# Optimization experiments

Hardware: AMD Instinct MI355X
Metric: run time of the kernel (lower is better)

The kernel has to match this reference:

```python
import jax, jax.numpy as jnp
import numpy as np

EPS = 1e-5

def layer_norm(x, g, b):
    m = x.mean(-1, keepdims=True)
    v = ((x - m) ** 2).mean(-1, keepdims=True)
    return (x - m) * jax.lax.rsqrt(v + EPS) * g + b

def setup_inputs() -> dict:
    key = jax.random.key(0)
    ks = jax.random.split(key, 12)
    H = 2048; E = 2048; I = 2048; N = 32
    A = (H + E) // 2  # attention hidden = 2048
    s = lambda fan: 1.0 / np.sqrt(fan)
    inp = {
        "input":   jax.random.normal(ks[0], (I,), jnp.float32),
        "hiddens": jax.random.normal(ks[1], (N, H), jnp.float32),
        "cells":   jax.random.normal(ks[2], (N, H), jnp.float32),
        "external":jax.random.normal(ks[3], (E,), jnp.float32),
        # weights (torch nn.Linear layout: [out, in]); LN enabled -> no biases on linears
        "W_ai":   jax.random.uniform(ks[4], (A, H + E), jnp.float32, -s(H+E), s(H+E)),
        "W_attn": jax.random.uniform(ks[5], (1, A), jnp.float32, -s(A), s(A)),
        "W_merge":jax.random.uniform(ks[6], (H, H), jnp.float32, -s(H), s(H)),
        "W_iou":  jax.random.uniform(ks[7], (3 * H, I + H), jnp.float32, -s(I+H), s(I+H)),
        "W_fi":   jax.random.uniform(ks[8], (H, I), jnp.float32, -s(I), s(I)),
        "W_fh":   jax.random.uniform(ks[9], (H, H), jnp.float32, -s(H), s(H)),
        "g_merge": jnp.ones((H,), jnp.float32), "b_merge": jnp.zeros((H,), jnp.float32),
        "g_f": jnp.ones((H,), jnp.float32), "b_f": jnp.zeros((H,), jnp.float32),
        "g_i": jnp.ones((H,), jnp.float32), "b_i": jnp.zeros((H,), jnp.float32),
        "g_o": jnp.ones((H,), jnp.float32), "b_o": jnp.zeros((H,), jnp.float32),
        "g_u": jnp.ones((H,), jnp.float32), "b_u": jnp.zeros((H,), jnp.float32),
        "g_c": jnp.ones((H,), jnp.float32), "b_c": jnp.zeros((H,), jnp.float32),
    }
    return inp

def reference(input, hiddens, cells, external,
              W_ai, W_attn, W_merge, W_iou, W_fi, W_fh,
              g_merge, b_merge, g_f, b_f, g_i, b_i, g_o, b_o, g_u, b_u, g_c, b_c):
    N, H = hiddens.shape
    # forget-gate preactivations: [H] + [N,H] -> [N,H]
    f_lin = input @ W_fi.T + hiddens @ W_fh.T
    # attentive merge over children
    ext = jnp.broadcast_to(external, (N, external.shape[0]))
    ai = jnp.tanh(jnp.concatenate([hiddens, ext], axis=1) @ W_ai.T)       # [N, (H+E)//2]
    attn = jax.nn.softmax(ai @ W_attn.T, axis=0)                          # [N, 1]
    merged = (hiddens * attn).sum(0)                                      # [H]
    merge_hidden = jnp.tanh(layer_norm(merged @ W_merge.T, g_merge, b_merge))
    # i/o/u gates from [input ; merged_hidden]
    iou = jnp.concatenate([input, merge_hidden]) @ W_iou.T                # [3H]
    i_l, o_l, u_l = jnp.split(iou, 3)
    f = jax.nn.sigmoid(layer_norm(f_lin, g_f, b_f))                       # [N,H]
    i = jax.nn.sigmoid(layer_norm(i_l, g_i, b_i))
    o = jax.nn.sigmoid(layer_norm(o_l, g_o, b_o))
    u = jnp.tanh(layer_norm(u_l, g_u, b_u))                               # dropout=0 -> identity
    new_cell = layer_norm(i * u + (f * cells).sum(0), g_c, b_c)           # [H]
    new_h = o * jnp.tanh(new_cell)
    return new_h, new_cell
```

## Files before the change

### kernel.cpp

```cpp
#include <hip/hip_runtime.h>
#include <hip/hip_bf16.h>

typedef __bf16 bf16_t;
typedef __attribute__((ext_vector_type(8))) __bf16 bf16x8;
typedef __attribute__((ext_vector_type(4))) float f32x4;

#define EPSF 1e-5f

#define CVT8(dst, s0, s1)                                                      \
    dst[0]=(bf16_t)s0.x; dst[1]=(bf16_t)s0.y; dst[2]=(bf16_t)s0.z; dst[3]=(bf16_t)s0.w; \
    dst[4]=(bf16_t)s1.x; dst[5]=(bf16_t)s1.y; dst[6]=(bf16_t)s1.z; dst[7]=(bf16_t)s1.w;

__global__ __launch_bounds__(256) void s1(
    const float* __restrict__ hiddens, const float* __restrict__ external,
    const float* __restrict__ input,
    const float* __restrict__ W_ai, const float* __restrict__ W_fh,
    const float* __restrict__ W_fi, const float* __restrict__ W_attn,
    float* __restrict__ lp, float* __restrict__ fh_out, float* __restrict__ fi_out)
{
    __shared__ __align__(16) float sm[2176];
    const int b    = blockIdx.x;
    const int tid  = threadIdx.x;
    const int wave = tid >> 6;
    const int lane = tid & 63;

    if (b < 256) {
        const bool is_ai = (b < 128);
        const int  jt    = is_ai ? b : b - 128;
        const int  l15   = lane & 15;
        const int  quad  = lane >> 4;
        const int  k0    = wave * 512;
        const int  wstride = is_ai ? 4096 : 2048;
        const float* W  = is_ai ? W_ai : W_fh;

        const float* ap0 = hiddens + (size_t)l15 * 2048 + quad * 8 + k0;
        const float* ap1 = ap0 + 16 * 2048;
        const float* bp  = W + (size_t)(jt * 16 + l15) * wstride + quad * 8 + k0;

        f32x4 acc0 = {0.f,0.f,0.f,0.f}, acc1 = {0.f,0.f,0.f,0.f};

        if (is_ai) {
            const float* ep = bp + 2048;
            const float* xp = external + quad * 8 + k0;
            float ejacc = 0.f;
            for (int k = 0; k < 512; k += 32) {
                float4 b0 = *(const float4*)(bp + k);
                float4 b1 = *(const float4*)(bp + k + 4);
                float4 a0 = *(const float4*)(ap0 + k);
                float4 a1 = *(const float4*)(ap0 + k + 4);
                float4 c0 = *(const float4*)(ap1 + k);
                float4 c1 = *(const float4*)(ap1 + k + 4);
                bf16x8 bv, av0, av1;
                CVT8(bv, b0, b1); CVT8(av0, a0, a1); CVT8(av1, c0, c1);
                acc0 = __builtin_amdgcn_mfma_f32_16x16x32_bf16(av0, bv, acc0, 0, 0, 0);
                acc1 = __builtin_amdgcn_mfma_f32_16x16x32_bf16(av1, bv, acc1, 0, 0, 0);
                float4 e0 = *(const float4*)(ep + k);
                float4 e1 = *(const float4*)(ep + k + 4);
                float4 x0 = *(const float4*)(xp + k);
                float4 x1 = *(const float4*)(xp + k + 4);
                ejacc += e0.x*x0.x + e0.y*x0.y + e0.z*x0.z + e0.w*x0.w
                       + e1.x*x1.x + e1.y*x1.y + e1.z*x1.z + e1.w*x1.w;
            }
            ejacc += __shfl_xor(ejacc, 16, 64);
            ejacc += __shfl_xor(ejacc, 32, 64);
            if (quad == 0) sm[2048 + wave * 16 + l15] = ejacc;
        } else {
            for (int k = 0; k < 512; k += 32) {
                float4 b0 = *(const float4*)(bp + k);
                float4 b1 = *(const float4*)(bp + k + 4);
                float4 a0 = *(const float4*)(ap0 + k);
                float4 a1 = *(const float4*)(ap0 + k + 4);
                float4 c0 = *(const float4*)(ap1 + k);
                float4 c1 = *(const float4*)(ap1 + k + 4);
                bf16x8 bv, av0, av1;
                CVT8(bv, b0, b1); CVT8(av0, a0, a1); CVT8(av1, c0, c1);
                acc0 = __builtin_amdgcn_mfma_f32_16x16x32_bf16(av0, bv, acc0, 0, 0, 0);
                acc1 = __builtin_amdgcn_mfma_f32_16x16x32_bf16(av1, bv, acc1, 0, 0, 0);
            }
        }

        #pragma unroll
        for (int r = 0; r < 4; ++r) {
            sm[wave * 512 +       (quad * 4 + r) * 16 + l15] = acc0[r];
            sm[wave * 512 + 256 + (quad * 4 + r) * 16 + l15] = acc1[r];
        }
        __syncthreads();

        int row = tid >> 4, col = tid & 15;
        float s0  = sm[row*16+col]      + sm[512+row*16+col]
                  + sm[1024+row*16+col] + sm[1536+row*16+col];
        float s1v = sm[256+row*16+col]  + sm[768+row*16+col]
                  + sm[1280+row*16+col] + sm[1792+row*16+col];

        if (is_ai) {
            float ej = sm[2048+col] + sm[2064+col] + sm[2080+col] + sm[2096+col];
            float wat = W_attn[jt * 16 + col];
            float lg0 = tanhf(s0  + ej) * wat;
            float lg1 = tanhf(s1v + ej) * wat;
            #pragma unroll
            for (int m = 1; m < 16; m <<= 1) {
                lg0 += __shfl_xor(lg0, m, 64);
                lg1 += __shfl_xor(lg1, m, 64);
            }
            if (col == 0) {
                lp[jt * 32 + row]      = lg0;
                lp[jt * 32 + 16 + row] = lg1;
            }
        } else {
            fh_out[(size_t)row * 2048 + jt * 16 + col]        = s0;
            fh_out[(size_t)(16 + row) * 2048 + jt * 16 + col] = s1v;
        }
    } else {
        int bb = b - 256;
        #pragma unroll
        for (int r = 0; r < 2; ++r) {
            int row = bb * 8 + wave * 2 + r;
            const float4* wp = (const float4*)(W_fi + (size_t)row * 2048) + lane;
            const float4* xp = (const float4*)input + lane;
            float a = 0.f;
            #pragma unroll
            for (int k = 0; k < 512; k += 64) {
                float4 w = wp[k], v = xp[k];
                a += w.x*v.x + w.y*v.y + w.z*v.z + w.w*v.w;
            }
            #pragma unroll
            for (int off = 32; off; off >>= 1) a += __shfl_down(a, off, 64);
            if (lane == 0) fi_out[row] = a;
        }
    }
}

__global__ __launch_bounds__(256) void s2(
    const float* __restrict__ lp, const float* __restrict__ hiddens,
    const float* __restrict__ W_merge,
    const float* __restrict__ fi, const float* __restrict__ fh,
    float* __restrict__ mm, float* __restrict__ frs)
{
    int b = blockIdx.x, t = threadIdx.x;
    if (b < 256) {
        __shared__ float lred[32][9];
        __shared__ float attnw[32];
        __shared__ __align__(16) float merged_s[2048];
        int n = t >> 3, sl = t & 7;
        float p = 0.f;
        #pragma unroll
        for (int m = 0; m < 16; ++m) p += lp[(sl * 16 + m) * 32 + n];
        lred[n][sl] = p;
        __syncthreads();
        if (t < 32) {
            float lg = 0.f;
            #pragma unroll
            for (int m = 0; m < 8; ++m) lg += lred[t][m];
            lred[t][8] = lg;
        }
        __syncthreads();
        if (t < 32) {
            float mx = -1e30f;
            for (int m = 0; m < 32; ++m) mx = fmaxf(mx, lred[m][8]);
            float ss = 0.f;
            for (int m = 0; m < 32; ++m) ss += expf(lred[m][8] - mx);
            attnw[t] = expf(lred[t][8] - mx) / ss;
        }
        __syncthreads();
        #pragma unroll
        for (int i = 0; i < 8; ++i) {
            int h = i * 256 + t;
            float acc = 0.f;
            #pragma unroll 8
            for (int n2 = 0; n2 < 32; ++n2) acc += attnw[n2] * hiddens[n2 * 2048 + h];
            merged_s[h] = acc;
        }
        __syncthreads();

        int wave = t >> 6, lane = t & 63;
        #pragma unroll
        for (int r = 0; r < 2; ++r) {
            int row = b * 8 + wave * 2 + r;
            const float4* wp = (const float4*)(W_merge + (size_t)row * 2048) + lane;
            const float4* xp = (const float4*)merged_s + lane;
            float a = 0.f;
            #pragma unroll
            for (int k = 0; k < 512; k += 64) {
                float4 w = wp[k], v = xp[k];
                a += w.x*v.x + w.y*v.y + w.z*v.z + w.w*v.w;
            }
            #pragma unroll
            for (int off = 32; off; off >>= 1) a += __shfl_down(a, off, 64);
            if (lane == 0) mm[row] = a;
        }
    } else {
        __shared__ float s1a[256], s2a[256];
        int n = b - 256;
        float sum = 0.f, sq = 0.f;
        #pragma unroll
        for (int i = 0; i < 8; ++i) {
            int h = t * 8 + i;
            float v = fi[h] + fh[n * 2048 + h];
            sum += v; sq += v * v;
        }
        s1a[t] = sum; s2a[t] = sq;
        __syncthreads();
        for (int off = 128; off; off >>= 1) {
            if (t < off) { s1a[t] += s1a[t + off]; s2a[t] += s2a[t + off]; }
            __syncthreads();
        }
        if (t == 0) {
            const float inv = 1.f / 2048.f;
            float mean = s1a[0] * inv;
            frs[n * 2]     = mean;
            frs[n * 2 + 1] = rsqrtf(s2a[0] * inv - mean * mean + EPSF);
        }
    }
}

__global__ __launch_bounds__(256) void s3(
    const float* __restrict__ W_iou, const float* __restrict__ mm,
    const float* __restrict__ input, const float* __restrict__ g_merge,
    const float* __restrict__ b_merge,
    const float* __restrict__ fi, const float* __restrict__ fh,
    const float* __restrict__ frs, const float* __restrict__ g_f,
    const float* __restrict__ b_f, const float* __restrict__ cells,
    float* __restrict__ iou, float* __restrict__ fc)
{
    int b = blockIdx.x, t = threadIdx.x;
    if (b < 512) {
        __shared__ __align__(16) float xcat[4096];
        __shared__ float s1a[256], s2a[256];
        float v[8]; float sum = 0.f, sq = 0.f;
        #pragma unroll
        for (int i = 0; i < 8; ++i) {
            v[i] = mm[t * 8 + i]; sum += v[i]; sq += v[i] * v[i];
        }
        s1a[t] = sum; s2a[t] = sq;
        __syncthreads();
        for (int off = 128; off; off >>= 1) {
            if (t < off) { s1a[t] += s1a[t + off]; s2a[t] += s2a[t + off]; }
            __syncthreads();
        }
        const float inv = 1.f / 2048.f;
        float mean = s1a[0] * inv;
        float r = rsqrtf(s2a[0] * inv - mean * mean + EPSF);
        #pragma unroll
        for (int i = 0; i < 8; ++i) {
            int h = t * 8 + i;
            xcat[h]        = input[h];
            xcat[2048 + h] = tanhf((v[i] - mean) * r * g_merge[h] + b_merge[h]);
        }
        __syncthreads();

        int wave = t >> 6, lane = t & 63;
        #pragma unroll
        for (int rr = 0; rr < 3; ++rr) {
            int row = b * 12 + wave * 3 + rr;
            const float4* wp = (const float4*)(W_iou + (size_t)row * 4096) + lane;
            const float4* xp = (const float4*)xcat + lane;
            float a = 0.f;
            #pragma unroll
            for (int k = 0; k < 1024; k += 64) {
                float4 w = wp[k], x = xp[k];
                a += w.x*x.x + w.y*x.y + w.z*x.z + w.w*x.w;
            }
            #pragma unroll
            for (int off = 32; off; off >>= 1) a += __shfl_down(a, off, 64);
            if (lane == 0) iou[row] = a;
        }
    } else {
        int h = (b - 512) * 256 + t;
        float g = g_f[h], bb = b_f[h], f_i = fi[h];
        float acc = 0.f;
        for (int n = 0; n < 32; ++n) {
            float v = (f_i + fh[n * 2048 + h] - frs[n * 2]) * frs[n * 2 + 1] * g + bb;
            acc += (1.f / (1.f + expf(-v))) * cells[n * 2048 + h];
        }
        fc[h] = acc;
    }
}

__global__ __launch_bounds__(256) void s4_tail(
    const float* __restrict__ iou, const float* __restrict__ fc,
    const float* __restrict__ gi, const float* __restrict__ bi,
    const float* __restrict__ go, const float* __restrict__ bo,
    const float* __restrict__ gu, const float* __restrict__ bu,
    const float* __restrict__ gc, const float* __restrict__ bc,
    float* __restrict__ out)
{
    __shared__ float sA[6][256];
    int t = threadIdx.x;
    float vi[8], vo[8], vu[8];
    float si = 0, qi = 0, so = 0, qo = 0, su = 0, qu = 0;
    #pragma unroll
    for (int i = 0; i < 8; ++i) {
        int h = t * 8 + i;
        vi[i] = iou[h]; vo[i] = iou[2048 + h]; vu[i] = iou[4096 + h];
        si += vi[i]; qi += vi[i] * vi[i];
        so += vo[i]; qo += vo[i] * vo[i];
        su += vu[i]; qu += vu[i] * vu[i];
    }
    sA[0][t] = si; sA[1][t] = qi; sA[2][t] = so;
    sA[3][t] = qo; sA[4][t] = su; sA[5][t] = qu;
    __syncthreads();
    for (int off = 128; off; off >>= 1) {
        if (t < off) {
            #pragma unroll
            for (int c = 0; c < 6; ++c) sA[c][t] += sA[c][t + off];
        }
        __syncthreads();
    }
    const float inv = 1.f / 2048.f;
    float mi = sA[0][0] * inv, ri = rsqrtf(sA[1][0] * inv - mi * mi + EPSF);
    float mo = sA[2][0] * inv, ro = rsqrtf(sA[3][0] * inv - mo * mo + EPSF);
    float mu = sA[4][0] * inv, ru = rsqrtf(sA[5][0] * inv - mu * mu + EPSF);
    __syncthreads();

    float o_[8], v_[8];
    float sv = 0, qv = 0;
    #pragma unroll
    for (int i = 0; i < 8; ++i) {
        int h = t * 8 + i;
        float ivl = 1.f / (1.f + expf(-((vi[i] - mi) * ri * gi[h] + bi[h])));
        o_[i]     = 1.f / (1.f + expf(-((vo[i] - mo) * ro * go[h] + bo[h])));
        float uvl = tanhf((vu[i] - mu) * ru * gu[h] + bu[h]);
        v_[i] = ivl * uvl + fc[h];
        sv += v_[i]; qv += v_[i] * v_[i];
    }
    sA[0][t] = sv; sA[1][t] = qv;
    __syncthreads();
    for (int off = 128; off; off >>= 1) {
        if (t < off) { sA[0][t] += sA[0][t + off]; sA[1][t] += sA[1][t + off]; }
        __syncthreads();
    }
    float mc = sA[0][0] * inv, rc = rsqrtf(sA[1][0] * inv - mc * mc + EPSF);
    #pragma unroll
    for (int i = 0; i < 8; ++i) {
        int h = t * 8 + i;
        float nc = (v_[i] - mc) * rc * gc[h] + bc[h];
        out[h]        = o_[i] * tanhf(nc);
        out[2048 + h] = nc;
    }
}

extern "C" void kernel_launch(void* const* d_in, const int* in_sizes, int n_in,
                              void* d_out, int out_size, void* d_ws, size_t ws_size,
                              hipStream_t stream)
{
    const float* input    = (const float*)d_in[0];
    const float* hiddens  = (const float*)d_in[1];
    const float* cells    = (const float*)d_in[2];
    const float* external = (const float*)d_in[3];
    const float* W_ai     = (const float*)d_in[4];
    const float* W_attn   = (const float*)d_in[5];
    const float* W_merge  = (const float*)d_in[6];
    const float* W_iou    = (const float*)d_in[7];
    const float* W_fi     = (const float*)d_in[8];
    const float* W_fh     = (const float*)d_in[9];
    const float* g_merge  = (const float*)d_in[10];
    const float* b_merge  = (const float*)d_in[11];
    const float* g_f      = (const float*)d_in[12];
    const float* b_f      = (const float*)d_in[13];
    const float* g_i      = (const float*)d_in[14];
    const float* b_i      = (const float*)d_in[15];
    const float* g_o      = (const float*)d_in[16];
    const float* b_o      = (const float*)d_in[17];
    const float* g_u      = (const float*)d_in[18];
    const float* b_u      = (const float*)d_in[19];
    const float* g_c      = (const float*)d_in[20];
    const float* b_c      = (const float*)d_in[21];

    float* ws = (float*)d_ws;
    float* ws_lp     = ws;
    float* ws_fh     = ws + 4096;
    float* ws_fi     = ws + 69632;
    float* ws_frs    = ws + 71680;
    float* ws_mm     = ws + 71744;
    float* ws_fc     = ws + 73792;
    float* ws_iou    = ws + 75840;
    float* out = (float*)d_out;

    s1<<<512, 256, 0, stream>>>(hiddens, external, input, W_ai, W_fh, W_fi,
                                W_attn, ws_lp, ws_fh, ws_fi);
    s2<<<288, 256, 0, stream>>>(ws_lp, hiddens, W_merge, ws_fi, ws_fh,
                                ws_mm, ws_frs);
    s3<<<520, 256, 0, stream>>>(W_iou, ws_mm, input, g_merge, b_merge,
                                ws_fi, ws_fh, ws_frs, g_f, b_f, cells,
                                ws_iou, ws_fc);
    s4_tail<<<1, 256, 0, stream>>>(ws_iou, ws_fc, g_i, b_i, g_o, b_o,
                                   g_u, b_u, g_c, b_c, out);
}
```

Baseline: 286.9 us.

## Split attention merge into its own kernel and regroup forget-gate stats

Before, each of the 256 W_merge GEMV blocks redid the softmax over attention logits and the full 32x2048 weighted sum of hiddens. That work now runs once in a new 8-block kernel that writes the merged vector to workspace, and the GEMV reads it from global memory. The forget-gate layer-norm statistics move into the W_merge kernel's side blocks. Each of the 8 fc blocks computes all 32 row statistics itself and then builds fc, so the W_iou kernel no longer carries the fc blocks. This adds one kernel launch and repeats the statistics eight times, serially over 32 rows within each block, which may lengthen the critical path.

After: 312.7 us. 9.0% more time.

```diff
diff --git a/kernel.cpp b/kernel.cpp
--- a/kernel.cpp
+++ b/kernel.cpp
@@ -11,7 +11,7 @@
     dst[0]=(bf16_t)s0.x; dst[1]=(bf16_t)s0.y; dst[2]=(bf16_t)s0.z; dst[3]=(bf16_t)s0.w; \
     dst[4]=(bf16_t)s1.x; dst[5]=(bf16_t)s1.y; dst[6]=(bf16_t)s1.z; dst[7]=(bf16_t)s1.w;
 
-__global__ __launch_bounds__(256) void s1(
+__global__ __launch_bounds__(256) void k1(
     const float* __restrict__ hiddens, const float* __restrict__ external,
     const float* __restrict__ input,
     const float* __restrict__ W_ai, const float* __restrict__ W_fh,
@@ -130,54 +130,56 @@
     }
 }
 
-__global__ __launch_bounds__(256) void s2(
+__global__ __launch_bounds__(256) void k2(
     const float* __restrict__ lp, const float* __restrict__ hiddens,
-    const float* __restrict__ W_merge,
+    float* __restrict__ merged)
+{
+    __shared__ float lred[32][9];
+    __shared__ float attnw[32];
+    int b = blockIdx.x, t = threadIdx.x;
+    int n = t >> 3, sl = t & 7;
+    float p = 0.f;
+    #pragma unroll
+    for (int m = 0; m < 16; ++m) p += lp[(sl * 16 + m) * 32 + n];
+    lred[n][sl] = p;
+    __syncthreads();
+    if (t < 32) {
+        float lg = 0.f;
+        #pragma unroll
+        for (int m = 0; m < 8; ++m) lg += lred[t][m];
+        lred[t][8] = lg;
+    }
+    __syncthreads();
+    if (t < 32) {
+        float mx = -1e30f;
+        for (int m = 0; m < 32; ++m) mx = fmaxf(mx, lred[m][8]);
+        float ss = 0.f;
+        for (int m = 0; m < 32; ++m) ss += expf(lred[m][8] - mx);
+        attnw[t] = expf(lred[t][8] - mx) / ss;
+    }
+    __syncthreads();
+    int h = b * 256 + t;
+    float acc = 0.f;
+    #pragma unroll 8
+    for (int n2 = 0; n2 < 32; ++n2) acc += attnw[n2] * hiddens[n2 * 2048 + h];
+    merged[h] = acc;
+}
+
+__global__ __launch_bounds__(256) void k3(
+    const float* __restrict__ W_merge, const float* __restrict__ merged,
     const float* __restrict__ fi, const float* __restrict__ fh,
-    float* __restrict__ mm, float* __restrict__ frs)
+    const float* __restrict__ g_f, const float* __restrict__ b_f,
+    const float* __restrict__ cells,
+    float* __restrict__ mm, float* __restrict__ fc)
 {
     int b = blockIdx.x, t = threadIdx.x;
     if (b < 256) {
-        __shared__ float lred[32][9];
-        __shared__ float attnw[32];
-        __shared__ __align__(16) float merged_s[2048];
-        int n = t >> 3, sl = t & 7;
-        float p = 0.f;
-        #pragma unroll
-        for (int m = 0; m < 16; ++m) p += lp[(sl * 16 + m) * 32 + n];
-        lred[n][sl] = p;
-        __syncthreads();
-        if (t < 32) {
-            float lg = 0.f;
-            #pragma unroll
-            for (int m = 0; m < 8; ++m) lg += lred[t][m];
-            lred[t][8] = lg;
-        }
-        __syncthreads();
-        if (t < 32) {
-            float mx = -1e30f;
-            for (int m = 0; m < 32; ++m) mx = fmaxf(mx, lred[m][8]);
-            float ss = 0.f;
-            for (int m = 0; m < 32; ++m) ss += expf(lred[m][8] - mx);
-            attnw[t] = expf(lred[t][8] - mx) / ss;
-        }
-        __syncthreads();
-        #pragma unroll
-        for (int i = 0; i < 8; ++i) {
-            int h = i * 256 + t;
-            float acc = 0.f;
-            #pragma unroll 8
-            for (int n2 = 0; n2 < 32; ++n2) acc += attnw[n2] * hiddens[n2 * 2048 + h];
-            merged_s[h] = acc;
-        }
-        __syncthreads();
-
         int wave = t >> 6, lane = t & 63;
         #pragma unroll
         for (int r = 0; r < 2; ++r) {
             int row = b * 8 + wave * 2 + r;
             const float4* wp = (const float4*)(W_merge + (size_t)row * 2048) + lane;
-            const float4* xp = (const float4*)merged_s + lane;
+            const float4* xp = (const float4*)merged + lane;
             float a = 0.f;
             #pragma unroll
             for (int k = 0; k < 512; k += 64) {
@@ -189,94 +191,91 @@
             if (lane == 0) mm[row] = a;
         }
     } else {
-        __shared__ float s1a[256], s2a[256];
-        int n = b - 256;
-        float sum = 0.f, sq = 0.f;
-        #pragma unroll
-        for (int i = 0; i < 8; ++i) {
-            int h = t * 8 + i;
-            float v = fi[h] + fh[n * 2048 + h];
-            sum += v; sq += v * v;
-        }
-        s1a[t] = sum; s2a[t] = sq;
-        __syncthreads();
-        for (int off = 128; off; off >>= 1) {
-            if (t < off) { s1a[t] += s1a[t + off]; s2a[t] += s2a[t + off]; }
+        __shared__ float r1[256], r2[256];
+        __shared__ float frs_s[64];
+        for (int n = 0; n < 32; ++n) {
+            float sum = 0.f, sq = 0.f;
+            #pragma unroll
+            for (int i = 0; i < 8; ++i) {
+                int h = t * 8 + i;
+                float v = fi[h] + fh[n * 2048 + h];
+                sum += v; sq += v * v;
+            }
+            r1[t] = sum; r2[t] = sq;
             __syncthreads();
-        }
-        if (t == 0) {
-            const float inv = 1.f / 2048.f;
-            float mean = s1a[0] * inv;
-            frs[n * 2]     = mean;
-            frs[n * 2 + 1] = rsqrtf(s2a[0] * inv - mean * mean + EPSF);
-        }
-    }
-}
-
-__global__ __launch_bounds__(256) void s3(
-    const float* __restrict__ W_iou, const float* __restrict__ mm,
-    const float* __restrict__ input, const float* __restrict__ g_merge,
-    const float* __restrict__ b_merge,
-    const float* __restrict__ fi, const float* __restrict__ fh,
-    const float* __restrict__ frs, const float* __restrict__ g_f,
-    const float* __restrict__ b_f, const float* __restrict__ cells,
-    float* __restrict__ iou, float* __restrict__ fc)
-{
-    int b = blockIdx.x, t = threadIdx.x;
-    if (b < 512) {
-        __shared__ __align__(16) float xcat[4096];
-        __shared__ float s1a[256], s2a[256];
-        float v[8]; float sum = 0.f, sq = 0.f;
-        #pragma unroll
-        for (int i = 0; i < 8; ++i) {
-            v[i] = mm[t * 8 + i]; sum += v[i]; sq += v[i] * v[i];
-        }
-        s1a[t] = sum; s2a[t] = sq;
-        __syncthreads();
-        for (int off = 128; off; off >>= 1) {
-            if (t < off) { s1a[t] += s1a[t + off]; s2a[t] += s2a[t + off]; }
+            for (int off = 128; off; off >>= 1) {
+                if (t < off) { r1[t] += r1[t + off]; r2[t] += r2[t + off]; }
+                __syncthreads();
+            }
+            if (t == 0) {
+                const float inv = 1.f / 2048.f;
+                float mean = r1[0] * inv;
+                frs_s[n * 2]     = mean;
+                frs_s[n * 2 + 1] = rsqrtf(r2[0] * inv - mean * mean + EPSF);
+            }
             __syncthreads();
         }
-        const float inv = 1.f / 2048.f;
-        float mean = s1a[0] * inv;
-        float r = rsqrtf(s2a[0] * inv - mean * mean + EPSF);
-        #pragma unroll
-        for (int i = 0; i < 8; ++i) {
-            int h = t * 8 + i;
-            xcat[h]        = input[h];
-            xcat[2048 + h] = tanhf((v[i] - mean) * r * g_merge[h] + b_merge[h]);
-        }
-        __syncthreads();
-
-        int wave = t >> 6, lane = t & 63;
-        #pragma unroll
-        for (int rr = 0; rr < 3; ++rr) {
-            int row = b * 12 + wave * 3 + rr;
-            const float4* wp = (const float4*)(W_iou + (size_t)row * 4096) + lane;
-            const float4* xp = (const float4*)xcat + lane;
-            float a = 0.f;
-            #pragma unroll
-            for (int k = 0; k < 1024; k += 64) {
-                float4 w = wp[k], x = xp[k];
-                a += w.x*x.x + w.y*x.y + w.z*x.z + w.w*x.w;
-            }
-            #pragma unroll
-            for (int off = 32; off; off >>= 1) a += __shfl_down(a, off, 64);
-            if (lane == 0) iou[row] = a;
-        }
-    } else {
-        int h = (b - 512) * 256 + t;
+        int h = (b - 256) * 256 + t;
         float g = g_f[h], bb = b_f[h], f_i = fi[h];
         float acc = 0.f;
         for (int n = 0; n < 32; ++n) {
-            float v = (f_i + fh[n * 2048 + h] - frs[n * 2]) * frs[n * 2 + 1] * g + bb;
+            float v = (f_i + fh[n * 2048 + h] - frs_s[n * 2]) * frs_s[n * 2 + 1] * g + bb;
             acc += (1.f / (1.f + expf(-v))) * cells[n * 2048 + h];
         }
         fc[h] = acc;
     }
 }
 
-__global__ __launch_bounds__(256) void s4_tail(
+__global__ __launch_bounds__(256) void k4(
+    const float* __restrict__ W_iou, const float* __restrict__ mm,
+    const float* __restrict__ input, const float* __restrict__ g_merge,
+    const float* __restrict__ b_merge, float* __restrict__ iou)
+{
+    __shared__ __align__(16) float xcat[4096];
+    __shared__ float s1a[256], s2a[256];
+    int b = blockIdx.x, t = threadIdx.x;
+
+    float v[8]; float sum = 0.f, sq = 0.f;
+    #pragma unroll
+    for (int i = 0; i < 8; ++i) {
+        v[i] = mm[t * 8 + i]; sum += v[i]; sq += v[i] * v[i];
+    }
+    s1a[t] = sum; s2a[t] = sq;
+    __syncthreads();
+    for (int off = 128; off; off >>= 1) {
+        if (t < off) { s1a[t] += s1a[t + off]; s2a[t] += s2a[t + off]; }
+        __syncthreads();
+    }
+    const float inv = 1.f / 2048.f;
+    float mean = s1a[0] * inv;
+    float r = rsqrtf(s2a[0] * inv - mean * mean + EPSF);
+    #pragma unroll
+    for (int i = 0; i < 8; ++i) {
+        int h = t * 8 + i;
+        xcat[h]        = input[h];
+        xcat[2048 + h] = tanhf((v[i] - mean) * r * g_merge[h] + b_merge[h]);
+    }
+    __syncthreads();
+
+    int wave = t >> 6, lane = t & 63;
+    #pragma unroll
+    for (int rr = 0; rr < 3; ++rr) {
+        int row = b * 12 + wave * 3 + rr;
+        const float4* wp = (const float4*)(W_iou + (size_t)row * 4096) + lane;
+        const float4* xp = (const float4*)xcat + lane;
+        float a = 0.f;
+        #pragma unroll
+        for (int k = 0; k < 1024; k += 64) {
+            float4 w = wp[k], x = xp[k];
+            a += w.x*x.x + w.y*x.y + w.z*x.z + w.w*x.w;
+        }
+        #pragma unroll
+        for (int off = 32; off; off >>= 1) a += __shfl_down(a, off, 64);
+        if (lane == 0) iou[row] = a;
+    }
+}
+
+__global__ __launch_bounds__(256) void k5_tail(
     const float* __restrict__ iou, const float* __restrict__ fc,
     const float* __restrict__ gi, const float* __restrict__ bi,
     const float* __restrict__ go, const float* __restrict__ bo,
@@ -370,19 +369,18 @@
     float* ws_lp     = ws;
     float* ws_fh     = ws + 4096;
     float* ws_fi     = ws + 69632;
-    float* ws_frs    = ws + 71680;
-    float* ws_mm     = ws + 71744;
-    float* ws_fc     = ws + 73792;
-    float* ws_iou    = ws + 75840;
+    float* ws_merged = ws + 71680;
+    float* ws_mm     = ws + 73728;
+    float* ws_fc     = ws + 75776;
+    float* ws_iou    = ws + 77824;
     float* out = (float*)d_out;
 
-    s1<<<512, 256, 0, stream>>>(hiddens, external, input, W_ai, W_fh, W_fi,
+    k1<<<512, 256, 0, stream>>>(hiddens, external, input, W_ai, W_fh, W_fi,
                                 W_attn, ws_lp, ws_fh, ws_fi);
-    s2<<<288, 256, 0, stream>>>(ws_lp, hiddens, W_merge, ws_fi, ws_fh,
-                                ws_mm, ws_frs);
-    s3<<<520, 256, 0, stream>>>(W_iou, ws_mm, input, g_merge, b_merge,
-                                ws_fi, ws_fh, ws_frs, g_f, b_f, cells,
-                                ws_iou, ws_fc);
-    s4_tail<<<1, 256, 0, stream>>>(ws_iou, ws_fc, g_i, b_i, g_o, b_o,
+    k2<<<8, 256, 0, stream>>>(ws_lp, hiddens, ws_merged);
+    k3<<<264, 256, 0, stream>>>(W_merge, ws_merged, ws_fi, ws_fh,
+                                g_f, b_f, cells, ws_mm, ws_fc);
+    k4<<<512, 256, 0, stream>>>(W_iou, ws_mm, input, g_merge, b_merge, ws_iou);
+    k5_tail<<<1, 256, 0, stream>>>(ws_iou, ws_fc, g_i, b_i, g_o, b_o,
                                    g_u, b_u, g_c, b_c, out);
 }
```
